# Kernel tuning notes

Hardware: AMD Instinct MI355X
Metric: run time of the kernel (lower is better)

Reference implementation:

```python
import jax, jax.numpy as jnp
import numpy as np

N, E, G = 50000, 800000, 50
H, D = 4, 64            # num_heads, h_dim
HD = H * D              # next_in_feats = 256
NODE_IN = 6 + 20        # node_s + seq embedding
NEG_SLOPE = 0.2


def setup_inputs() -> dict:
    key = jax.random.key(0)
    ks = jax.random.split(key, 16)
    # graph structure: random edges + self loops so every node has in-degree >= 1
    src = jnp.concatenate([jax.random.randint(ks[0], (E - N,), 0, N), jnp.arange(N)]).astype(jnp.int32)
    dst = jnp.concatenate([jax.random.randint(ks[1], (E - N,), 0, N), jnp.arange(N)]).astype(jnp.int32)
    graph_id = (jnp.arange(N) // (N // G)).astype(jnp.int32)  # 50 graphs of 1000 nodes
    s = 0.05
    inp = {
        'seq': jax.random.randint(ks[2], (N,), 0, 20),
        'node_s': jax.random.normal(ks[3], (N, 6), jnp.float32),
        'src': src, 'dst': dst, 'graph_id': graph_id,
        'W_emb': jax.random.normal(ks[4], (20, 20), jnp.float32) * s,
        'W0': jax.random.normal(ks[5], (NODE_IN, HD), jnp.float32) * s,
        'al0': jax.random.normal(ks[6], (H, D), jnp.float32) * s,
        'ar0': jax.random.normal(ks[7], (H, D), jnp.float32) * s,
        'b0': jnp.zeros((HD,), jnp.float32),
        'W1': jax.random.normal(ks[8], (HD, HD), jnp.float32) * s,
        'al1': jax.random.normal(ks[9], (H, D), jnp.float32) * s,
        'ar1': jax.random.normal(ks[10], (H, D), jnp.float32) * s,
        'b1': jnp.zeros((HD,), jnp.float32),
        'W2': jax.random.normal(ks[11], (HD, HD), jnp.float32) * s,
        'al2': jax.random.normal(ks[12], (H, D), jnp.float32) * s,
        'ar2': jax.random.normal(ks[13], (H, D), jnp.float32) * s,
        'b2': jnp.zeros((HD,), jnp.float32),
        'Wd1': jax.random.normal(ks[14], (HD, 512), jnp.float32) * s,
        'bd1': jnp.zeros((512,), jnp.float32),
        'Wd2': jax.random.normal(ks[15], (512, 1), jnp.float32) * s,
        'bd2': jnp.zeros((1,), jnp.float32),
    }
    return inp


def gat_layer(h, W, al, ar, b, src, dst):
    ft = (h @ W).reshape(N, H, D)                    # [N,H,D]
    el = jnp.einsum('nhd,hd->nh', ft, al)            # src-side score
    er = jnp.einsum('nhd,hd->nh', ft, ar)            # dst-side score
    e = jax.nn.leaky_relu(el[src] + er[dst], NEG_SLOPE)  # [E,H]
    m = jax.lax.stop_gradient(jax.ops.segment_max(e, dst, num_segments=N))
    ee = jnp.exp(e - m[dst])
    z = jax.ops.segment_sum(ee, dst, num_segments=N)     # [N,H]
    alpha = ee / z[dst]                                   # edge softmax over dst
    msg = ft[src] * alpha[:, :, None]                     # [E,H,D]
    out = jax.ops.segment_sum(msg, dst, num_segments=N)   # [N,H,D]
    return out.reshape(N, HD) + b


def reference(seq, node_s, src, dst, graph_id, W_emb, W0, al0, ar0, b0,
              W1, al1, ar1, b1, W2, al2, ar2, b2, Wd1, bd1, Wd2, bd2):
    h = jnp.concatenate([W_emb[seq], node_s], axis=1)     # [N,26]
    h = gat_layer(h, W0, al0, ar0, b0, src, dst)
    h = gat_layer(h, W1, al1, ar1, b1, src, dst)
    h = gat_layer(h, W2, al2, ar2, b2, src, dst)
    h = jax.nn.relu(h)                                    # dropout in eval mode = identity
    out = jax.nn.relu(h @ Wd1 + bd1) @ Wd2 + bd2 + 0.5    # [N,1]
    cnt = jax.ops.segment_sum(jnp.ones((N,), out.dtype), graph_id, num_segments=G)
    g_out = jax.ops.segment_sum(out, graph_id, num_segments=G) / cnt[:, None]  # [G,1]
    return out, g_out
```

## Files before the change

kernel.cpp:

```cpp
#include <hip/hip_runtime.h>
#include <hip/hip_bf16.h>
#include <float.h>

#define NN 50000
#define EE 800000
#define GG 50
#define HH 4
#define DD 64
#define HD 256
#define NODE_IN 26
#define NEG_SLOPE 0.2f
#define SCAN_NB ((NN + 255) / 256)
#define PB 128

typedef __attribute__((ext_vector_type(8))) short short8v;
typedef __attribute__((ext_vector_type(4))) float floatx4;

static __device__ __forceinline__ ushort f2bf(float f) {
    __hip_bfloat16 b = __float2bfloat16(f);
    return *(ushort*)&b;
}

static __device__ __forceinline__ float bf2f(ushort u) {
    return __uint_as_float(((unsigned)u) << 16);
}

static __device__ __forceinline__ float lrelu(float e) {
    return (e >= 0.f) ? e : NEG_SLOPE * e;
}

__global__ void embed_bf16_kernel(const int* __restrict__ seq,
                                  const float* __restrict__ node_s,
                                  const float* __restrict__ W_emb,
                                  ushort* __restrict__ hbf) {
    int idx = blockIdx.x * blockDim.x + threadIdx.x;
    if (idx >= NN * 32) return;
    int n = idx >> 5;
    int j = idx & 31;
    float v = 0.f;
    if (j < 20)      v = W_emb[seq[n] * 20 + j];
    else if (j < 26) v = node_s[n * 6 + (j - 20)];
    hbf[idx] = f2bf(v);
}

__global__ void wtrans_kernel(const float* __restrict__ W,
                              ushort* __restrict__ Wt,
                              int K, int N, int Kp) {
    int idx = blockIdx.x * blockDim.x + threadIdx.x;
    if (idx >= N * Kp) return;
    int n = idx / Kp;
    int k = idx - n * Kp;
    float v = (k < K) ? W[(size_t)k * N + n] : 0.f;
    Wt[idx] = f2bf(v);
}

__global__ __launch_bounds__(256) void gemm_mfma_kernel(
    const ushort* __restrict__ A, const ushort* __restrict__ Bt,
    ushort* __restrict__ Cbf, float* __restrict__ Cf,
    const float* __restrict__ bias,
    const float* __restrict__ al, const float* __restrict__ ar,
    float* __restrict__ el, float* __restrict__ er,
    int M, int N, int Kp, int relu_out) {
    __shared__ ushort As[128][40];
    __shared__ ushort Bs[64][40];

    int tid  = threadIdx.x;
    int wave = tid >> 6;
    int lane = tid & 63;
    int bm = blockIdx.y * 128;
    int bn = blockIdx.x * 64;

    floatx4 acc[2][4];
    #pragma unroll
    for (int i = 0; i < 2; ++i)
        #pragma unroll
        for (int j = 0; j < 4; ++j)
            acc[i][j] = (floatx4){0.f, 0.f, 0.f, 0.f};

    const int lr = lane & 15;
    const int lk = (lane >> 4) * 8;
    const int lq = lane >> 4;

    for (int k0 = 0; k0 < Kp; k0 += 32) {
        #pragma unroll
        for (int p = 0; p < 2; ++p) {
            int idx = p * 256 + tid;
            int r = idx >> 2, kk = (idx & 3) * 8;
            int gr = bm + r;
            short8v v = {};
            if (gr < M) v = *(const short8v*)(A + (size_t)gr * Kp + k0 + kk);
            *(short8v*)(&As[r][kk]) = v;
        }
        {
            int c = tid >> 2, kk = (tid & 3) * 8;
            short8v v = *(const short8v*)(Bt + (size_t)(bn + c) * Kp + k0 + kk);
            *(short8v*)(&Bs[c][kk]) = v;
        }
        __syncthreads();

        short8v bfrag[4];
        #pragma unroll
        for (int cs = 0; cs < 4; ++cs)
            bfrag[cs] = *(const short8v*)(&Bs[cs * 16 + lr][lk]);
        #pragma unroll
        for (int rs = 0; rs < 2; ++rs) {
            short8v afrag = *(const short8v*)(&As[wave * 32 + rs * 16 + lr][lk]);
            #pragma unroll
            for (int cs = 0; cs < 4; ++cs)
                acc[rs][cs] = __builtin_amdgcn_mfma_f32_16x16x32_bf16(
                    afrag, bfrag[cs], acc[rs][cs], 0, 0, 0);
        }
        __syncthreads();
    }

    const int h_blk = bn >> 6;
    float alv[4], arv[4];
    if (al) {
        #pragma unroll
        for (int cs = 0; cs < 4; ++cs) {
            alv[cs] = al[h_blk * DD + cs * 16 + lr];
            arv[cs] = ar[h_blk * DD + cs * 16 + lr];
        }
    }

    #pragma unroll
    for (int rs = 0; rs < 2; ++rs)
        #pragma unroll
        for (int j = 0; j < 4; ++j) {
            int row = bm + wave * 32 + rs * 16 + lq * 4 + j;
            if (row >= M) continue;
            float sl = 0.f, sr = 0.f;
            #pragma unroll
            for (int cs = 0; cs < 4; ++cs) {
                float raw = acc[rs][cs][j];
                float v = raw;
                int col = bn + cs * 16 + lr;
                if (bias) v += bias[col];
                if (relu_out) v = fmaxf(v, 0.f);
                if (Cbf) Cbf[(size_t)row * N + col] = f2bf(v);
                else     Cf [(size_t)row * N + col] = v;
                if (al) {
                    sl = fmaf(raw, alv[cs], sl);
                    sr = fmaf(raw, arv[cs], sr);
                }
            }
            if (al) {
                #pragma unroll
                for (int off = 1; off < 16; off <<= 1) {
                    sl += __shfl_xor(sl, off);
                    sr += __shfl_xor(sr, off);
                }
                if (lr == 0) {
                    el[row * HH + h_blk] = sl;
                    er[row * HH + h_blk] = sr;
                }
            }
        }
}

__global__ void hist_kernel(const int* __restrict__ dst, int* __restrict__ cnt) {
    for (int i = blockIdx.x * blockDim.x + threadIdx.x; i < EE;
         i += gridDim.x * blockDim.x)
        atomicAdd(&cnt[dst[i]], 1);
}

__global__ __launch_bounds__(256) void scan_partial_kernel(
    const int* __restrict__ cnt, int* __restrict__ bsum) {
    __shared__ int s[256];
    int b = blockIdx.x, t = threadIdx.x;
    int i = b * 256 + t;
    s[t] = (i < NN) ? cnt[i] : 0;
    __syncthreads();
    for (int off = 128; off; off >>= 1) {
        if (t < off) s[t] += s[t + off];
        __syncthreads();
    }
    if (t == 0) bsum[b] = s[0];
}

__global__ __launch_bounds__(256) void scan_bsums_kernel(
    const int* __restrict__ bsum, int* __restrict__ boff) {
    __shared__ int s[256];
    int t = threadIdx.x;
    int v = (t < SCAN_NB) ? bsum[t] : 0;
    s[t] = v;
    __syncthreads();
    #pragma unroll
    for (int off = 1; off < 256; off <<= 1) {
        int u = (t >= off) ? s[t - off] : 0;
        __syncthreads();
        s[t] += u;
        __syncthreads();
    }
    if (t < SCAN_NB) boff[t] = s[t] - v;
}

__global__ __launch_bounds__(256) void scan_final_kernel(
    const int* __restrict__ cnt, const int* __restrict__ boff,
    int* __restrict__ rowptr) {
    __shared__ int s[256];
    int b = blockIdx.x, t = threadIdx.x;
    int i = b * 256 + t;
    int v = (i < NN) ? cnt[i] : 0;
    s[t] = v;
    __syncthreads();
    #pragma unroll
    for (int off = 1; off < 256; off <<= 1) {
        int u = (t >= off) ? s[t - off] : 0;
        __syncthreads();
        s[t] += u;
        __syncthreads();
    }
    int incl = s[t] + boff[b];
    if (i < NN) rowptr[i] = incl - v;
    if (i == NN - 1) rowptr[NN] = incl;
}

__global__ void scatter_kernel(const int* __restrict__ src,
                               const int* __restrict__ dst,
                               const int* __restrict__ rowptr,
                               int* __restrict__ fill,
                               int* __restrict__ colsrc) {
    for (int i = blockIdx.x * blockDim.x + threadIdx.x; i < EE;
         i += gridDim.x * blockDim.x) {
        int d = dst[i];
        int pos = atomicAdd(&fill[d], 1);
        colsrc[rowptr[d] + pos] = src[i];
    }
}

__global__ __launch_bounds__(256) void aggregate_kernel(
    const ushort* __restrict__ ft, const float* __restrict__ el,
    const float* __restrict__ er, const int* __restrict__ rowptr,
    const int* __restrict__ colsrc, const float* __restrict__ bias,
    ushort* __restrict__ out, int relu_out) {
    __shared__ float4 plds[4][64];
    __shared__ int    slds[4][64];

    int v = (blockIdx.x * blockDim.x + threadIdx.x) >> 6;
    int lane = threadIdx.x & 63;
    int w = threadIdx.x >> 6;
    if (v >= NN) return;
    int base = rowptr[v];
    int deg = rowptr[v + 1] - base;

    const int h = lane >> 4;
    float4 er4 = ((const float4*)er)[v];

    float z0 = 0.f, z1 = 0.f, z2 = 0.f, z3 = 0.f;
    float4 acc = {0.f, 0.f, 0.f, 0.f};
    const float* pf = (const float*)plds[w];

    for (int c = 0; c < deg; c += 64) {
        int clen = min(64, deg - c);
        if (lane < clen) {
            int s_j = colsrc[base + c + lane];
            float4 el4 = ((const float4*)el)[s_j];
            float p0 = expf(lrelu(el4.x + er4.x));
            float p1 = expf(lrelu(el4.y + er4.y));
            float p2 = expf(lrelu(el4.z + er4.z));
            float p3 = expf(lrelu(el4.w + er4.w));
            z0 += p0; z1 += p1; z2 += p2; z3 += p3;
            slds[w][lane] = s_j;
            plds[w][lane] = (float4){p0, p1, p2, p3};
        }
        #pragma unroll 8
        for (int jj = 0; jj < clen; ++jj) {
            int   s = slds[w][jj];
            float q = pf[jj * 4 + h];
            ushort4 f4 = ((const ushort4*)(ft + (size_t)s * HD))[lane];
            acc.x = fmaf(q, bf2f(f4.x), acc.x);
            acc.y = fmaf(q, bf2f(f4.y), acc.y);
            acc.z = fmaf(q, bf2f(f4.z), acc.z);
            acc.w = fmaf(q, bf2f(f4.w), acc.w);
        }
    }

    #pragma unroll
    for (int off = 32; off; off >>= 1) {
        z0 += __shfl_xor(z0, off);
        z1 += __shfl_xor(z1, off);
        z2 += __shfl_xor(z2, off);
        z3 += __shfl_xor(z3, off);
    }
    float zh = (h < 2) ? ((h == 0) ? z0 : z1) : ((h == 2) ? z2 : z3);
    float zi = 1.f / zh;

    float4 b4 = ((const float4*)bias)[lane];
    float o0 = acc.x * zi + b4.x;
    float o1 = acc.y * zi + b4.y;
    float o2 = acc.z * zi + b4.z;
    float o3 = acc.w * zi + b4.w;
    if (relu_out) {
        o0 = fmaxf(o0, 0.f); o1 = fmaxf(o1, 0.f);
        o2 = fmaxf(o2, 0.f); o3 = fmaxf(o3, 0.f);
    }
    ushort4 st = {f2bf(o0), f2bf(o1), f2bf(o2), f2bf(o3)};
    *(ushort4*)(out + (size_t)v * HD + lane * 4) = st;
}

__global__ __launch_bounds__(256) void final_kernel(
    const float* __restrict__ hidden, const float* __restrict__ Wd2,
    const float* __restrict__ bd2, float* __restrict__ out) {
    int n = (blockIdx.x * blockDim.x + threadIdx.x) >> 6;
    int lane = threadIdx.x & 63;
    if (n >= NN) return;
    const float4* hr = (const float4*)(hidden + (size_t)n * 512);
    const float4* w  = (const float4*)Wd2;
    float4 a0 = hr[lane];
    float4 a1 = hr[lane + 64];
    float4 w0 = w[lane];
    float4 w1 = w[lane + 64];
    float s = a0.x * w0.x + a0.y * w0.y + a0.z * w0.z + a0.w * w0.w
            + a1.x * w1.x + a1.y * w1.y + a1.z * w1.z + a1.w * w1.w;
    #pragma unroll
    for (int off = 32; off; off >>= 1) s += __shfl_xor(s, off);
    if (lane == 0) out[n] = s + bd2[0] + 0.5f;
}

__global__ __launch_bounds__(256) void pool_partial_kernel(
    const float* __restrict__ out, const int* __restrict__ graph_id,
    float* __restrict__ psum, float* __restrict__ pcnt) {
    __shared__ float ls[64], lc[64];
    int b = blockIdx.x, t = threadIdx.x;
    if (t < 64) { ls[t] = 0.f; lc[t] = 0.f; }
    __syncthreads();
    for (int n = b * 256 + t; n < NN; n += PB * 256) {
        int g = graph_id[n];
        atomicAdd(&ls[g], out[n]);
        atomicAdd(&lc[g], 1.f);
    }
    __syncthreads();
    if (t < GG) {
        psum[t * PB + b] = ls[t];
        pcnt[t * PB + b] = lc[t];
    }
}

__global__ __launch_bounds__(256) void pool_final_kernel(
    const float* __restrict__ psum, const float* __restrict__ pcnt,
    float* __restrict__ gout) {
    int g = (blockIdx.x * blockDim.x + threadIdx.x) >> 6;
    int lane = threadIdx.x & 63;
    if (g >= GG) return;
    float s = psum[g * PB + lane] + psum[g * PB + 64 + lane];
    float c = pcnt[g * PB + lane] + pcnt[g * PB + 64 + lane];
    #pragma unroll
    for (int off = 32; off; off >>= 1) {
        s += __shfl_xor(s, off);
        c += __shfl_xor(c, off);
    }
    if (lane == 0) gout[g] = s / c;
}

static inline size_t align_up(size_t x, size_t a) { return (x + a - 1) & ~(a - 1); }

extern "C" void kernel_launch(void* const* d_in, const int* in_sizes, int n_in,
                              void* d_out, int out_size, void* d_ws, size_t ws_size,
                              hipStream_t stream) {
    const int*   seq    = (const int*)d_in[0];
    const float* node_s = (const float*)d_in[1];
    const int*   src    = (const int*)d_in[2];
    const int*   dst    = (const int*)d_in[3];
    const int*   graph_id = (const int*)d_in[4];
    const float* W_emb  = (const float*)d_in[5];
    const float* W0     = (const float*)d_in[6];
    const float* al0    = (const float*)d_in[7];
    const float* ar0    = (const float*)d_in[8];
    const float* b0     = (const float*)d_in[9];
    const float* W1     = (const float*)d_in[10];
    const float* al1    = (const float*)d_in[11];
    const float* ar1    = (const float*)d_in[12];
    const float* b1     = (const float*)d_in[13];
    const float* W2     = (const float*)d_in[14];
    const float* al2    = (const float*)d_in[15];
    const float* ar2    = (const float*)d_in[16];
    const float* b2     = (const float*)d_in[17];
    const float* Wd1    = (const float*)d_in[18];
    const float* bd1    = (const float*)d_in[19];
    const float* Wd2    = (const float*)d_in[20];
    const float* bd2    = (const float*)d_in[21];

    float* out_nodes  = (float*)d_out;
    float* out_graphs = (float*)d_out + NN;

    char* p = (char*)d_ws;
    size_t off = 0;
    auto alloc = [&](size_t bytes) {
        void* r = p + off;
        off = align_up(off + bytes, 256);
        return r;
    };
    ushort* ftbf  = (ushort*)alloc((size_t)NN * HD * 2);
    float*  hidden= (float*)alloc((size_t)NN * 512 * 4);
    ushort* hbf0  = (ushort*)alloc((size_t)NN * 32 * 2);
    ushort* hbuf  = (ushort*)alloc((size_t)NN * HD * 2);
    float*  el    = (float*)alloc((size_t)NN * HH * 4);
    float*  er    = (float*)alloc((size_t)NN * HH * 4);
    int*    rowptr= (int*)alloc((size_t)(NN + 1) * 4);
    int*    fill  = (int*)alloc((size_t)NN * 4);
    int*    colsrc= (int*)alloc((size_t)EE * 4);
    int*    bsum  = (int*)alloc(256 * 4);
    int*    boff  = (int*)alloc(256 * 4);
    float*  psum  = (float*)alloc((size_t)64 * PB * 4);
    float*  pcnt  = (float*)alloc((size_t)64 * PB * 4);
    ushort* Wt0   = (ushort*)alloc((size_t)HD * 32 * 2);
    ushort* Wt1   = (ushort*)alloc((size_t)HD * HD * 2);
    ushort* Wt2   = (ushort*)alloc((size_t)HD * HD * 2);
    ushort* Wtd1  = (ushort*)alloc((size_t)512 * HD * 2);
    (void)ws_size;

    hipMemsetAsync(fill, 0, (size_t)NN * 4, stream);
    hist_kernel<<<1024, 256, 0, stream>>>(dst, fill);
    scan_partial_kernel<<<SCAN_NB, 256, 0, stream>>>(fill, bsum);
    scan_bsums_kernel<<<1, 256, 0, stream>>>(bsum, boff);
    scan_final_kernel<<<SCAN_NB, 256, 0, stream>>>(fill, boff, rowptr);
    hipMemsetAsync(fill, 0, (size_t)NN * 4, stream);
    scatter_kernel<<<1024, 256, 0, stream>>>(src, dst, rowptr, fill, colsrc);

    wtrans_kernel<<<(HD * 32 + 255) / 256, 256, 0, stream>>>(W0, Wt0, NODE_IN, HD, 32);
    wtrans_kernel<<<(HD * HD + 255) / 256, 256, 0, stream>>>(W1, Wt1, HD, HD, HD);
    wtrans_kernel<<<(HD * HD + 255) / 256, 256, 0, stream>>>(W2, Wt2, HD, HD, HD);
    wtrans_kernel<<<(512 * HD + 255) / 256, 256, 0, stream>>>(Wd1, Wtd1, HD, 512, HD);

    embed_bf16_kernel<<<(NN * 32 + 255) / 256, 256, 0, stream>>>(seq, node_s, W_emb, hbf0);

    const int nodeWaves = (NN * 64 + 255) / 256;
    dim3 gemm256(256 / 64, (NN + 127) / 128);
    dim3 gemm512(512 / 64, (NN + 127) / 128);

    gemm_mfma_kernel<<<gemm256, 256, 0, stream>>>(hbf0, Wt0, ftbf, nullptr, nullptr,
                                                  al0, ar0, el, er, NN, HD, 32, 0);
    aggregate_kernel<<<nodeWaves, 256, 0, stream>>>(ftbf, el, er, rowptr, colsrc, b0, hbuf, 0);

    gemm_mfma_kernel<<<gemm256, 256, 0, stream>>>(hbuf, Wt1, ftbf, nullptr, nullptr,
                                                  al1, ar1, el, er, NN, HD, HD, 0);
    aggregate_kernel<<<nodeWaves, 256, 0, stream>>>(ftbf, el, er, rowptr, colsrc, b1, hbuf, 0);

    gemm_mfma_kernel<<<gemm256, 256, 0, stream>>>(hbuf, Wt2, ftbf, nullptr, nullptr,
                                                  al2, ar2, el, er, NN, HD, HD, 0);
    aggregate_kernel<<<nodeWaves, 256, 0, stream>>>(ftbf, el, er, rowptr, colsrc, b2, hbuf, 1);

    gemm_mfma_kernel<<<gemm512, 256, 0, stream>>>(hbuf, Wtd1, nullptr, hidden, bd1,
                                                  nullptr, nullptr, nullptr, nullptr,
                                                  NN, 512, HD, 1);
    final_kernel<<<nodeWaves, 256, 0, stream>>>(hidden, Wd2, bd2, out_nodes);
    pool_partial_kernel<<<PB, 256, 0, stream>>>(out_nodes, graph_id, psum, pcnt);
    pool_final_kernel<<<(GG * 64 + 255) / 256, 256, 0, stream>>>(psum, pcnt, out_graphs);
}
```

Baseline: 558.2 us.

## Widen GEMM block tile to 256 columns so A tiles load once per row block

Each GEMM block now covers 256 output columns (all four heads) instead of 64. This means each 128-row A tile is staged into shared memory once rather than four times, and one block computes el/er for all heads. The cost is 32 accumulator fragments per thread and a larger shared B tile, which raises register pressure and lowers occupancy. The grid also shrinks to about 391 blocks for the 256-column GEMMs.

```diff
diff --git a/kernel.cpp b/kernel.cpp
--- a/kernel.cpp
+++ b/kernel.cpp
@@ -62,19 +62,19 @@
     float* __restrict__ el, float* __restrict__ er,
     int M, int N, int Kp, int relu_out) {
     __shared__ ushort As[128][40];
-    __shared__ ushort Bs[64][40];
+    __shared__ ushort Bs[256][40];
 
     int tid  = threadIdx.x;
     int wave = tid >> 6;
     int lane = tid & 63;
     int bm = blockIdx.y * 128;
-    int bn = blockIdx.x * 64;
-
-    floatx4 acc[2][4];
+    int bn = blockIdx.x * 256;
+
+    floatx4 acc[2][16];
     #pragma unroll
     for (int i = 0; i < 2; ++i)
         #pragma unroll
-        for (int j = 0; j < 4; ++j)
+        for (int j = 0; j < 16; ++j)
             acc[i][j] = (floatx4){0.f, 0.f, 0.f, 0.f};
 
     const int lr = lane & 15;
@@ -91,35 +91,34 @@
             if (gr < M) v = *(const short8v*)(A + (size_t)gr * Kp + k0 + kk);
             *(short8v*)(&As[r][kk]) = v;
         }
-        {
-            int c = tid >> 2, kk = (tid & 3) * 8;
+        #pragma unroll
+        for (int p = 0; p < 4; ++p) {
+            int idx = p * 256 + tid;
+            int c = idx >> 2, kk = (idx & 3) * 8;
             short8v v = *(const short8v*)(Bt + (size_t)(bn + c) * Kp + k0 + kk);
             *(short8v*)(&Bs[c][kk]) = v;
         }
         __syncthreads();
 
-        short8v bfrag[4];
-        #pragma unroll
-        for (int cs = 0; cs < 4; ++cs)
-            bfrag[cs] = *(const short8v*)(&Bs[cs * 16 + lr][lk]);
         #pragma unroll
         for (int rs = 0; rs < 2; ++rs) {
             short8v afrag = *(const short8v*)(&As[wave * 32 + rs * 16 + lr][lk]);
             #pragma unroll
-            for (int cs = 0; cs < 4; ++cs)
+            for (int cs = 0; cs < 16; ++cs) {
+                short8v bfrag = *(const short8v*)(&Bs[cs * 16 + lr][lk]);
                 acc[rs][cs] = __builtin_amdgcn_mfma_f32_16x16x32_bf16(
-                    afrag, bfrag[cs], acc[rs][cs], 0, 0, 0);
-        }
-        __syncthreads();
-    }
-
-    const int h_blk = bn >> 6;
-    float alv[4], arv[4];
+                    afrag, bfrag, acc[rs][cs], 0, 0, 0);
+            }
+        }
+        __syncthreads();
+    }
+
+    float alv[16], arv[16];
     if (al) {
         #pragma unroll
-        for (int cs = 0; cs < 4; ++cs) {
-            alv[cs] = al[h_blk * DD + cs * 16 + lr];
-            arv[cs] = ar[h_blk * DD + cs * 16 + lr];
+        for (int cs = 0; cs < 16; ++cs) {
+            alv[cs] = al[cs * 16 + lr];
+            arv[cs] = ar[cs * 16 + lr];
         }
     }
 
@@ -129,9 +128,10 @@
         for (int j = 0; j < 4; ++j) {
             int row = bm + wave * 32 + rs * 16 + lq * 4 + j;
             if (row >= M) continue;
-            float sl = 0.f, sr = 0.f;
+            float sl[HH] = {0.f, 0.f, 0.f, 0.f};
+            float sr[HH] = {0.f, 0.f, 0.f, 0.f};
             #pragma unroll
-            for (int cs = 0; cs < 4; ++cs) {
+            for (int cs = 0; cs < 16; ++cs) {
                 float raw = acc[rs][cs][j];
                 float v = raw;
                 int col = bn + cs * 16 + lr;
@@ -140,19 +140,25 @@
                 if (Cbf) Cbf[(size_t)row * N + col] = f2bf(v);
                 else     Cf [(size_t)row * N + col] = v;
                 if (al) {
-                    sl = fmaf(raw, alv[cs], sl);
-                    sr = fmaf(raw, arv[cs], sr);
+                    sl[cs >> 2] = fmaf(raw, alv[cs], sl[cs >> 2]);
+                    sr[cs >> 2] = fmaf(raw, arv[cs], sr[cs >> 2]);
                 }
             }
             if (al) {
                 #pragma unroll
                 for (int off = 1; off < 16; off <<= 1) {
-                    sl += __shfl_xor(sl, off);
-                    sr += __shfl_xor(sr, off);
+                    #pragma unroll
+                    for (int h = 0; h < HH; ++h) {
+                        sl[h] += __shfl_xor(sl[h], off);
+                        sr[h] += __shfl_xor(sr[h], off);
+                    }
                 }
                 if (lr == 0) {
-                    el[row * HH + h_blk] = sl;
-                    er[row * HH + h_blk] = sr;
+                    #pragma unroll
+                    for (int h = 0; h < HH; ++h) {
+                        el[row * HH + h] = sl[h];
+                        er[row * HH + h] = sr[h];
+                    }
                 }
             }
         }
@@ -426,8 +432,8 @@
     embed_bf16_kernel<<<(NN * 32 + 255) / 256, 256, 0, stream>>>(seq, node_s, W_emb, hbf0);
 
     const int nodeWaves = (NN * 64 + 255) / 256;
-    dim3 gemm256(256 / 64, (NN + 127) / 128);
-    dim3 gemm512(512 / 64, (NN + 127) / 128);
+    dim3 gemm256(1, (NN + 127) / 128);
+    dim3 gemm512(2, (NN + 127) / 128);
 
     gemm_mfma_kernel<<<gemm256, 256, 0, stream>>>(hbf0, Wt0, ftbf, nullptr, nullptr,
                                                   al0, ar0, el, er, NN, HD, 32, 0);
```

New measurement: 671.9 us. 20.4% more time.
